# Performance work log

Measured on AMD Instinct MI355X. Metric: run time of the kernel, lower is better.

## Reference

```python
import jax, jax.numpy as jnp
import numpy as np

DIMS = [14400, 7200, 3600, 1800, 900, 450]  # in_dim then floor(dim/2) per layer
K = 25
BATCH = 256
NSTEPS = 10
OUT_DIM = 2


def setup_inputs() -> dict:
    key = jax.random.key(0)
    ks = jax.random.split(key, 13)
    inp = {"input": jax.random.normal(ks[0], (BATCH, NSTEPS, DIMS[0]), dtype=jnp.float32)}
    w_scale = (2.0 / K) ** 0.5  # matches normal_(0, (2/K)**0.5) init
    for i in range(5):
        d_prev, d = DIMS[i], DIMS[i + 1]
        inp[f"knn{i}"] = jax.random.randint(ks[1 + i], (d, K), 0, d_prev)
        inp[f"w{i}"] = w_scale * jax.random.normal(ks[6 + i], (d, K), dtype=jnp.float32)
        inp[f"b{i}"] = jnp.zeros((1, d), dtype=jnp.float32)
    inp["fc_w"] = jax.random.normal(ks[11], (OUT_DIM, DIMS[-1]), dtype=jnp.float32) * (1.0 / DIMS[-1] ** 0.5)
    inp["fc_b"] = jnp.zeros((OUT_DIM,), dtype=jnp.float32)
    return inp


def reference(input, knn0, knn1, knn2, knn3, knn4,
              w0, w1, w2, w3, w4, b0, b1, b2, b3, b4, fc_w, fc_b):
    # Faithful to the torch module: the synapses/membranes dicts are never
    # reassigned inside the step loop, so every snntorch Synaptic call sees
    # zero state: reset = Heaviside(0 - thr) = 0, syn = alpha*0 + I = I,
    # mem = beta*0 + syn = I.  The returned mem (x) is therefore exactly the
    # layer drive, there is no cross-step recurrence, and `angles` is
    # overwritten each step, so only the final timestep reaches the output.
    knns = (knn0, knn1, knn2, knn3, knn4)
    ws = (w0, w1, w2, w3, w4)
    bs = (b0, b1, b2, b3, b4)
    x = input[:, -1, :]  # [B, in_dim] -- last step (permute(1,0,2) then input[step])
    for knn, w, b in zip(knns, ws, bs):
        # gather KNN inputs [B, dim, K], weight locally, reduce over K, add bias
        x = jnp.einsum('bdk,dk->bd', x[:, knn], w) + b
    angles = x @ fc_w.T + fc_b  # fc_angle
    return angles  # (mem4_rec, spk4_rec are empty lists in the original)
```

## Files before the change

kernel.cpp:

```cpp
#include <hip/hip_runtime.h>
#include <hip/hip_fp16.h>

#define NSTEPS 10
#define D_IN   14400
#define KNN_K  25

#define L0D 7200
#define L1D 3600
#define L2D 1800
#define L3D 900
#define L4D 450
#define NROWS 13950

#define G0 113
#define G1 57
#define G2 29
#define G3 15
#define G4 8
#define SPG 832
#define O1 (G0*SPG)
#define O2 (O1 + G1*SPG)
#define O3 (O2 + G2*SPG)
#define O4 (O3 + G3*SPG)
#define OTOT (O4 + G4*SPG)

#define NPAIR 128
#define NPACK (NPAIR * (D_IN/4))

#define SPLIT0 3584
#define SPLIT1 1792

__device__ __forceinline__ unsigned f16b(float x) {
    return (unsigned)__half_as_ushort(__float2half_rn(x));
}

__device__ __forceinline__ void gh2(unsigned u, const char* __restrict__ actb,
                                    float& s0, float& s1) {
    const __half2 av = *(const __half2*)(actb + (u & 0xffffu));
    const __half  wh = __ushort_as_half((unsigned short)(u >> 16));
    s0 = fmaf(__half2float(__low2half(av)),  __half2float(wh), s0);
    s1 = fmaf(__half2float(__high2half(av)), __half2float(wh), s1);
}

__global__ void prep_kernel(const int* __restrict__ k0, const float* __restrict__ w0,
                            const int* __restrict__ k1, const float* __restrict__ w1,
                            const int* __restrict__ k2, const float* __restrict__ w2,
                            const int* __restrict__ k3, const float* __restrict__ w3,
                            const int* __restrict__ k4, const float* __restrict__ w4,
                            const float* __restrict__ input,
                            uint2* __restrict__ tile, uint4* __restrict__ xpk)
{
    const int s = blockIdx.x * 256 + threadIdx.x;
    if (s < NROWS) {
        const int* kp; const float* wp; int dl, obase;
        if      (s < L0D)             { kp = k0; wp = w0; dl = s;             obase = 0;  }
        else if (s < L0D+L1D)         { kp = k1; wp = w1; dl = s - L0D;       obase = O1; }
        else if (s < L0D+L1D+L2D)     { kp = k2; wp = w2; dl = s-L0D-L1D;     obase = O2; }
        else if (s < L0D+L1D+L2D+L3D) { kp = k3; wp = w3; dl = s-L0D-L1D-L2D; obase = O3; }
        else                          { kp = k4; wp = w4; dl = s-L0D-L1D-L2D-L3D; obase = O4; }
        const int g = dl >> 6, l = dl & 63;

        int idx[KNN_K]; float wv[KNN_K]; int bk[KNN_K];
#pragma unroll
        for (int k = 0; k < KNN_K; ++k) {
            idx[k] = kp[dl * KNN_K + k];
            wv[k]  = wp[dl * KNN_K + k];
            bk[k]  = idx[k] & 31;
        }
        const int lm = l - (l >= 50 ? 50 : (l >= 25 ? 25 : 0));
        unsigned* tw = (unsigned*)tile + 2u * (unsigned)(obase + g * SPG);
#pragma unroll
        for (int k = 0; k < KNN_K; ++k) {
            int rank = 0;
#pragma unroll
            for (int j = 0; j < KNN_K; ++j)
                rank += (bk[j] < bk[k]) || (bk[j] == bk[k] && j < k);
            int slot = rank + lm; if (slot >= KNN_K) slot -= KNN_K;
            unsigned u = (f16b(wv[k]) << 16) | ((unsigned)idx[k] << 2);
            tw[((slot >> 1) * 64 + l) * 2 + (slot & 1)] = u;
        }
        tw[(12 * 64 + l) * 2 + 1] = 0;
        return;
    }
    const int t = s - NROWS;
    if (t < NPACK) {
        const int p = t / (D_IN / 4);
        const int c = t - p * (D_IN / 4);
        const float4 a = *(const float4*)(input + ((size_t)(2*p)   * NSTEPS + NSTEPS-1) * D_IN + 4*c);
        const float4 b = *(const float4*)(input + ((size_t)(2*p+1) * NSTEPS + NSTEPS-1) * D_IN + 4*c);
        uint4 wd;
        wd.x = f16b(a.x) | (f16b(b.x) << 16);
        wd.y = f16b(a.y) | (f16b(b.y) << 16);
        wd.z = f16b(a.z) | (f16b(b.z) << 16);
        wd.w = f16b(a.w) | (f16b(b.w) << 16);
        xpk[(size_t)p * (D_IN / 4) + c] = wd;
    }
}

template<int MAXI, int BLK>
__device__ __forceinline__ void glayerG(const char* __restrict__ actb,
                                        unsigned* __restrict__ yout,
                                        const uint2* __restrict__ tb,
                                        const float* __restrict__ bias,
                                        int lo, int hi, int tid)
{
#pragma unroll
    for (int i = 0; i < MAXI; ++i) {
        int r = lo + tid + i * BLK;
        if (r < hi) {
            const uint2* tp = tb + (size_t)(r >> 6) * SPG + (r & 63);
            float a0 = bias[r], a1 = a0, c0 = 0.f, c1 = 0.f;
#pragma unroll
            for (int j = 0; j < 13; ++j) {
                uint2 u = tp[j * 64];
                gh2(u.x, actb, a0, a1);
                gh2(u.y, actb, c0, c1);
            }
            a0 += c0; a1 += c1;
            yout[r] = f16b(a0) | (f16b(a1) << 16);
        }
    }
}

__global__ __launch_bounds__(512, 2)
void lcn_l0(const uint4* __restrict__ xpk, const uint2* __restrict__ tile,
            const float* __restrict__ b0, unsigned* __restrict__ y0)
{
    __shared__ unsigned act[D_IN];
    const int tid = threadIdx.x;
    const int p   = blockIdx.x & 127;
    const int h   = blockIdx.x >> 7;

    const uint4* src = xpk + (size_t)p * (D_IN / 4);
    for (int i = tid; i < D_IN / 4; i += 512)
        *(uint4*)(act + 4 * i) = src[i];
    __syncthreads();

    glayerG<8, 512>((const char*)act, y0 + (size_t)p * L0D, tile, b0,
                    h ? SPLIT0 : 0, h ? L0D : SPLIT0, tid);
}

__global__ __launch_bounds__(512, 2)
void lcn_l1(const unsigned* __restrict__ y0, const uint2* __restrict__ tile,
            const float* __restrict__ b1, unsigned* __restrict__ y1)
{
    __shared__ unsigned act[L0D];
    const int tid = threadIdx.x;
    const int p   = blockIdx.x & 127;
    const int h   = blockIdx.x >> 7;

    const uint4* src = (const uint4*)(y0 + (size_t)p * L0D);
    for (int i = tid; i < L0D / 4; i += 512)
        *(uint4*)(act + 4 * i) = src[i];
    __syncthreads();

    glayerG<4, 512>((const char*)act, y1 + (size_t)p * L1D, tile + O1, b1,
                    h ? SPLIT1 : 0, h ? L1D : SPLIT1, tid);
}

__global__ __launch_bounds__(1024)
void lcn_tail(const unsigned* __restrict__ y1, const uint2* __restrict__ tile,
              const float* __restrict__ b2, const float* __restrict__ b3,
              const float* __restrict__ b4,
              const float* __restrict__ fc_w, const float* __restrict__ fc_b,
              float* __restrict__ out)
{
    __shared__ unsigned sm[L1D + L2D + L3D];
    __shared__ float y4[L4D];
    const int tid = threadIdx.x;
    const int p   = blockIdx.x & 127;
    const int h   = blockIdx.x >> 7;

    const uint4* src = (const uint4*)(y1 + (size_t)p * L1D);
    if (tid < L1D / 4) *(uint4*)(sm + 4 * tid) = src[tid];
    __syncthreads();

    glayerG<2, 1024>((const char*)sm, sm + L1D, tile + O2, b2, 0, L2D, tid);
    __syncthreads();
    glayerG<1, 1024>((const char*)(sm + L1D), sm + L1D + L2D, tile + O3, b3, 0, L3D, tid);
    __syncthreads();
    if (tid < L4D) {
        const uint2* tp = tile + O4 + (size_t)(tid >> 6) * SPG + (tid & 63);
        const char* actb = (const char*)(sm + L1D + L2D);
        float a0 = b4[tid], a1 = a0, c0 = 0.f, c1 = 0.f;
#pragma unroll
        for (int j = 0; j < 13; ++j) {
            uint2 u = tp[j * 64];
            gh2(u.x, actb, a0, a1);
            gh2(u.y, actb, c0, c1);
        }
        a0 += c0; a1 += c1;
        y4[tid] = h ? a1 : a0;
    }
    __syncthreads();

    if (tid < 128) {
        const int o = tid >> 6, lane = tid & 63;
        float s = 0.f;
#pragma unroll
        for (int it = 0; it < 8; ++it) {
            int r = lane + it * 64;
            if (r < L4D) s += y4[r] * fc_w[o * L4D + r];
        }
#pragma unroll
        for (int off = 32; off > 0; off >>= 1) s += __shfl_xor(s, off);
        if (lane == 0) out[(2 * p + h) * 2 + o] = s + fc_b[o];
    }
}

extern "C" void kernel_launch(void* const* d_in, const int* in_sizes, int n_in,
                              void* d_out, int out_size, void* d_ws, size_t ws_size,
                              hipStream_t stream) {
    const float* input = (const float*)d_in[0];
    const int*   knn[5];
    const float* w[5];
    const float* bias[5];
    for (int i = 0; i < 5; ++i) {
        knn[i]  = (const int*)  d_in[1 + 3 * i];
        w[i]    = (const float*)d_in[2 + 3 * i];
        bias[i] = (const float*)d_in[3 + 3 * i];
    }
    const float* fc_w = (const float*)d_in[16];
    const float* fc_b = (const float*)d_in[17];
    float* out = (float*)d_out;

    char* base = (char*)d_ws;
    uint2*    tile = (uint2*)base;
    uint4*    xpk  = (uint4*)(base + (size_t)OTOT * 8);
    unsigned* y0   = (unsigned*)((char*)xpk + (size_t)NPAIR * D_IN * 4);
    unsigned* y1   = y0 + (size_t)NPAIR * L0D;

    const int nprep = NROWS + NPACK;
    prep_kernel<<<(nprep + 255) / 256, 256, 0, stream>>>(
        knn[0], w[0], knn[1], w[1], knn[2], w[2], knn[3], w[3], knn[4], w[4],
        input, tile, xpk);

    lcn_l0<<<256, 512, 0, stream>>>(xpk, tile, bias[0], y0);
    lcn_l1<<<256, 512, 0, stream>>>(y0, tile, bias[1], y1);
    lcn_tail<<<256, 1024, 0, stream>>>(y1, tile, bias[2], bias[3], bias[4],
                                       fc_w, fc_b, out);
}
```

Measured before the change: 42.00 us.

## Fuse all LCN layers and input packing into one monolithic per-pair kernel

Replaces the three layer kernels and the input-packing part of the prep kernel with a single kernel. Each 1024-thread block loads one batch pair, converts it to packed fp16 in shared memory, runs all five layers from shared memory using ping-pong buffers, then computes the FC output. This removes the global round trips for the packed input and the y0/y1 intermediates, and cuts two kernel launches. In exchange the grid drops from 256 blocks to 128 blocks using about 86 KB of LDS each, which halves available parallelism and leaves part of the GPU idle.

```diff
diff --git a/kernel.cpp b/kernel.cpp
--- a/kernel.cpp
+++ b/kernel.cpp
@@ -25,10 +25,6 @@
 #define OTOT (O4 + G4*SPG)
 
 #define NPAIR 128
-#define NPACK (NPAIR * (D_IN/4))
-
-#define SPLIT0 3584
-#define SPLIT1 1792
 
 __device__ __forceinline__ unsigned f16b(float x) {
     return (unsigned)__half_as_ushort(__float2half_rn(x));
@@ -47,142 +43,50 @@
                             const int* __restrict__ k2, const float* __restrict__ w2,
                             const int* __restrict__ k3, const float* __restrict__ w3,
                             const int* __restrict__ k4, const float* __restrict__ w4,
-                            const float* __restrict__ input,
-                            uint2* __restrict__ tile, uint4* __restrict__ xpk)
+                            uint2* __restrict__ tile)
 {
     const int s = blockIdx.x * 256 + threadIdx.x;
-    if (s < NROWS) {
-        const int* kp; const float* wp; int dl, obase;
-        if      (s < L0D)             { kp = k0; wp = w0; dl = s;             obase = 0;  }
-        else if (s < L0D+L1D)         { kp = k1; wp = w1; dl = s - L0D;       obase = O1; }
-        else if (s < L0D+L1D+L2D)     { kp = k2; wp = w2; dl = s-L0D-L1D;     obase = O2; }
-        else if (s < L0D+L1D+L2D+L3D) { kp = k3; wp = w3; dl = s-L0D-L1D-L2D; obase = O3; }
-        else                          { kp = k4; wp = w4; dl = s-L0D-L1D-L2D-L3D; obase = O4; }
-        const int g = dl >> 6, l = dl & 63;
+    if (s >= NROWS) return;
+    const int* kp; const float* wp; int dl, obase;
+    if      (s < L0D)             { kp = k0; wp = w0; dl = s;             obase = 0;  }
+    else if (s < L0D+L1D)         { kp = k1; wp = w1; dl = s - L0D;       obase = O1; }
+    else if (s < L0D+L1D+L2D)     { kp = k2; wp = w2; dl = s-L0D-L1D;     obase = O2; }
+    else if (s < L0D+L1D+L2D+L3D) { kp = k3; wp = w3; dl = s-L0D-L1D-L2D; obase = O3; }
+    else                          { kp = k4; wp = w4; dl = s-L0D-L1D-L2D-L3D; obase = O4; }
+    const int g = dl >> 6, l = dl & 63;
 
-        int idx[KNN_K]; float wv[KNN_K]; int bk[KNN_K];
+    int idx[KNN_K]; float wv[KNN_K]; int bk[KNN_K];
 #pragma unroll
-        for (int k = 0; k < KNN_K; ++k) {
-            idx[k] = kp[dl * KNN_K + k];
-            wv[k]  = wp[dl * KNN_K + k];
-            bk[k]  = idx[k] & 31;
-        }
-        const int lm = l - (l >= 50 ? 50 : (l >= 25 ? 25 : 0));
-        unsigned* tw = (unsigned*)tile + 2u * (unsigned)(obase + g * SPG);
+    for (int k = 0; k < KNN_K; ++k) {
+        idx[k] = kp[dl * KNN_K + k];
+        wv[k]  = wp[dl * KNN_K + k];
+        bk[k]  = idx[k] & 31;
+    }
+    const int lm = l - (l >= 50 ? 50 : (l >= 25 ? 25 : 0));
+    unsigned* tw = (unsigned*)tile + 2u * (unsigned)(obase + g * SPG);
 #pragma unroll
-        for (int k = 0; k < KNN_K; ++k) {
-            int rank = 0;
+    for (int k = 0; k < KNN_K; ++k) {
+        int rank = 0;
 #pragma unroll
-            for (int j = 0; j < KNN_K; ++j)
-                rank += (bk[j] < bk[k]) || (bk[j] == bk[k] && j < k);
-            int slot = rank + lm; if (slot >= KNN_K) slot -= KNN_K;
-            unsigned u = (f16b(wv[k]) << 16) | ((unsigned)idx[k] << 2);
-            tw[((slot >> 1) * 64 + l) * 2 + (slot & 1)] = u;
-        }
-        tw[(12 * 64 + l) * 2 + 1] = 0;
-        return;
+        for (int j = 0; j < KNN_K; ++j)
+            rank += (bk[j] < bk[k]) || (bk[j] == bk[k] && j < k);
+        int slot = rank + lm; if (slot >= KNN_K) slot -= KNN_K;
+        unsigned u = (f16b(wv[k]) << 16) | ((unsigned)idx[k] << 2);
+        tw[((slot >> 1) * 64 + l) * 2 + (slot & 1)] = u;
     }
-    const int t = s - NROWS;
-    if (t < NPACK) {
-        const int p = t / (D_IN / 4);
-        const int c = t - p * (D_IN / 4);
-        const float4 a = *(const float4*)(input + ((size_t)(2*p)   * NSTEPS + NSTEPS-1) * D_IN + 4*c);
-        const float4 b = *(const float4*)(input + ((size_t)(2*p+1) * NSTEPS + NSTEPS-1) * D_IN + 4*c);
-        uint4 wd;
-        wd.x = f16b(a.x) | (f16b(b.x) << 16);
-        wd.y = f16b(a.y) | (f16b(b.y) << 16);
-        wd.z = f16b(a.z) | (f16b(b.z) << 16);
-        wd.w = f16b(a.w) | (f16b(b.w) << 16);
-        xpk[(size_t)p * (D_IN / 4) + c] = wd;
-    }
+    tw[(12 * 64 + l) * 2 + 1] = 0;
 }
 
-template<int MAXI, int BLK>
-__device__ __forceinline__ void glayerG(const char* __restrict__ actb,
-                                        unsigned* __restrict__ yout,
-                                        const uint2* __restrict__ tb,
-                                        const float* __restrict__ bias,
-                                        int lo, int hi, int tid)
+template<int DIM>
+__device__ __forceinline__ void glayer(const unsigned* __restrict__ actw,
+                                       unsigned* __restrict__ yout,
+                                       const uint2* __restrict__ tb,
+                                       const float* __restrict__ bias, int tid)
 {
-#pragma unroll
-    for (int i = 0; i < MAXI; ++i) {
-        int r = lo + tid + i * BLK;
-        if (r < hi) {
-            const uint2* tp = tb + (size_t)(r >> 6) * SPG + (r & 63);
-            float a0 = bias[r], a1 = a0, c0 = 0.f, c1 = 0.f;
-#pragma unroll
-            for (int j = 0; j < 13; ++j) {
-                uint2 u = tp[j * 64];
-                gh2(u.x, actb, a0, a1);
-                gh2(u.y, actb, c0, c1);
-            }
-            a0 += c0; a1 += c1;
-            yout[r] = f16b(a0) | (f16b(a1) << 16);
-        }
-    }
-}
-
-__global__ __launch_bounds__(512, 2)
-void lcn_l0(const uint4* __restrict__ xpk, const uint2* __restrict__ tile,
-            const float* __restrict__ b0, unsigned* __restrict__ y0)
-{
-    __shared__ unsigned act[D_IN];
-    const int tid = threadIdx.x;
-    const int p   = blockIdx.x & 127;
-    const int h   = blockIdx.x >> 7;
-
-    const uint4* src = xpk + (size_t)p * (D_IN / 4);
-    for (int i = tid; i < D_IN / 4; i += 512)
-        *(uint4*)(act + 4 * i) = src[i];
-    __syncthreads();
-
-    glayerG<8, 512>((const char*)act, y0 + (size_t)p * L0D, tile, b0,
-                    h ? SPLIT0 : 0, h ? L0D : SPLIT0, tid);
-}
-
-__global__ __launch_bounds__(512, 2)
-void lcn_l1(const unsigned* __restrict__ y0, const uint2* __restrict__ tile,
-            const float* __restrict__ b1, unsigned* __restrict__ y1)
-{
-    __shared__ unsigned act[L0D];
-    const int tid = threadIdx.x;
-    const int p   = blockIdx.x & 127;
-    const int h   = blockIdx.x >> 7;
-
-    const uint4* src = (const uint4*)(y0 + (size_t)p * L0D);
-    for (int i = tid; i < L0D / 4; i += 512)
-        *(uint4*)(act + 4 * i) = src[i];
-    __syncthreads();
-
-    glayerG<4, 512>((const char*)act, y1 + (size_t)p * L1D, tile + O1, b1,
-                    h ? SPLIT1 : 0, h ? L1D : SPLIT1, tid);
-}
-
-__global__ __launch_bounds__(1024)
-void lcn_tail(const unsigned* __restrict__ y1, const uint2* __restrict__ tile,
-              const float* __restrict__ b2, const float* __restrict__ b3,
-              const float* __restrict__ b4,
-              const float* __restrict__ fc_w, const float* __restrict__ fc_b,
-              float* __restrict__ out)
-{
-    __shared__ unsigned sm[L1D + L2D + L3D];
-    __shared__ float y4[L4D];
-    const int tid = threadIdx.x;
-    const int p   = blockIdx.x & 127;
-    const int h   = blockIdx.x >> 7;
-
-    const uint4* src = (const uint4*)(y1 + (size_t)p * L1D);
-    if (tid < L1D / 4) *(uint4*)(sm + 4 * tid) = src[tid];
-    __syncthreads();
-
-    glayerG<2, 1024>((const char*)sm, sm + L1D, tile + O2, b2, 0, L2D, tid);
-    __syncthreads();
-    glayerG<1, 1024>((const char*)(sm + L1D), sm + L1D + L2D, tile + O3, b3, 0, L3D, tid);
-    __syncthreads();
-    if (tid < L4D) {
-        const uint2* tp = tile + O4 + (size_t)(tid >> 6) * SPG + (tid & 63);
-        const char* actb = (const char*)(sm + L1D + L2D);
-        float a0 = b4[tid], a1 = a0, c0 = 0.f, c1 = 0.f;
+    const char* actb = (const char*)actw;
+    for (int r = tid; r < DIM; r += 1024) {
+        const uint2* tp = tb + (size_t)(r >> 6) * SPG + (r & 63);
+        float a0 = bias[r], a1 = a0, c0 = 0.f, c1 = 0.f;
 #pragma unroll
         for (int j = 0; j < 13; ++j) {
             uint2 u = tp[j * 64];
@@ -190,21 +94,68 @@
             gh2(u.y, actb, c0, c1);
         }
         a0 += c0; a1 += c1;
-        y4[tid] = h ? a1 : a0;
+        yout[r] = f16b(a0) | (f16b(a1) << 16);
+    }
+    __syncthreads();
+}
+
+__global__ __launch_bounds__(1024, 1)
+void lcn_mono(const float* __restrict__ input, const uint2* __restrict__ tile,
+              const float* __restrict__ b0, const float* __restrict__ b1,
+              const float* __restrict__ b2, const float* __restrict__ b3,
+              const float* __restrict__ b4,
+              const float* __restrict__ fc_w, const float* __restrict__ fc_b,
+              float* __restrict__ out)
+{
+    __shared__ unsigned sm[D_IN + L0D];
+    unsigned* X  = sm;
+    unsigned* Y0 = sm + D_IN;
+    unsigned* Y1 = sm;
+    unsigned* Y2 = sm + 3600;
+    unsigned* Y3 = sm + 5400;
+    unsigned* Y4 = sm + 6300;
+
+    const int tid = threadIdx.x;
+    const int p   = blockIdx.x;
+
+    {
+        const float4* r0 = (const float4*)(input + ((size_t)(2 * p)     * NSTEPS + NSTEPS - 1) * D_IN);
+        const float4* r1 = (const float4*)(input + ((size_t)(2 * p + 1) * NSTEPS + NSTEPS - 1) * D_IN);
+        for (int i = tid; i < D_IN / 4; i += 1024) {
+            float4 a = r0[i], b = r1[i];
+            uint4 wd;
+            wd.x = f16b(a.x) | (f16b(b.x) << 16);
+            wd.y = f16b(a.y) | (f16b(b.y) << 16);
+            wd.z = f16b(a.z) | (f16b(b.z) << 16);
+            wd.w = f16b(a.w) | (f16b(b.w) << 16);
+            *(uint4*)(X + 4 * i) = wd;
+        }
     }
     __syncthreads();
 
-    if (tid < 128) {
-        const int o = tid >> 6, lane = tid & 63;
+    glayer<L0D>(X,  Y0, tile,      b0, tid);
+    glayer<L1D>(Y0, Y1, tile + O1, b1, tid);
+    glayer<L2D>(Y1, Y2, tile + O2, b2, tid);
+    glayer<L3D>(Y2, Y3, tile + O3, b3, tid);
+    glayer<L4D>(Y3, Y4, tile + O4, b4, tid);
+
+    if (tid < 256) {
+        const int wv = tid >> 6, lane = tid & 63;
+        const int o = wv >> 1, j = wv & 1;
         float s = 0.f;
 #pragma unroll
         for (int it = 0; it < 8; ++it) {
             int r = lane + it * 64;
-            if (r < L4D) s += y4[r] * fc_w[o * L4D + r];
+            if (r < L4D) {
+                unsigned av = Y4[r];
+                const __half2 h2 = *(const __half2*)&av;
+                float xv = __half2float(j ? __high2half(h2) : __low2half(h2));
+                s += xv * fc_w[o * L4D + r];
+            }
         }
 #pragma unroll
         for (int off = 32; off > 0; off >>= 1) s += __shfl_xor(s, off);
-        if (lane == 0) out[(2 * p + h) * 2 + o] = s + fc_b[o];
+        if (lane == 0) out[(2 * p + j) * 2 + o] = s + fc_b[o];
     }
 }
 
@@ -224,19 +175,12 @@
     const float* fc_b = (const float*)d_in[17];
     float* out = (float*)d_out;
 
-    char* base = (char*)d_ws;
-    uint2*    tile = (uint2*)base;
-    uint4*    xpk  = (uint4*)(base + (size_t)OTOT * 8);
-    unsigned* y0   = (unsigned*)((char*)xpk + (size_t)NPAIR * D_IN * 4);
-    unsigned* y1   = y0 + (size_t)NPAIR * L0D;
+    uint2* tile = (uint2*)d_ws;
 
-    const int nprep = NROWS + NPACK;
-    prep_kernel<<<(nprep + 255) / 256, 256, 0, stream>>>(
-        knn[0], w[0], knn[1], w[1], knn[2], w[2], knn[3], w[3], knn[4], w[4],
-        input, tile, xpk);
+    prep_kernel<<<(NROWS + 255) / 256, 256, 0, stream>>>(
+        knn[0], w[0], knn[1], w[1], knn[2], w[2], knn[3], w[3], knn[4], w[4], tile);
 
-    lcn_l0<<<256, 512, 0, stream>>>(xpk, tile, bias[0], y0);
-    lcn_l1<<<256, 512, 0, stream>>>(y0, tile, bias[1], y1);
-    lcn_tail<<<256, 1024, 0, stream>>>(y1, tile, bias[2], bias[3], bias[4],
-                                       fc_w, fc_b, out);
+    lcn_mono<<<NPAIR, 1024, 0, stream>>>(
+        input, tile, bias[0], bias[1], bias[2], bias[3], bias[4],
+        fc_w, fc_b, out);
 }
```

Result: faster. 40.42 us (-3.8%).
